# Optimization experiments

Measured on AMD Instinct MI355X. Metric: run time of the kernel, lower is better.

## Reference

```python
import jax, jax.numpy as jnp
import numpy as np

TEMPERATURE = 0.1  # from __init__ temperature
NEG_INF = -1e30


def setup_inputs() -> dict:
    key = jax.random.key(0)
    k1, k2, k3, k4, k5 = jax.random.split(key, 5)
    B, D = 8192, 128
    return {
        "zis": jax.random.normal(k1, (B, D), dtype=jnp.float32),
        "zjs": jax.random.normal(k2, (B, D), dtype=jnp.float32),
        "ilabels": jax.random.randint(k3, (B,), 0, 100, dtype=jnp.int64),
        "jlabels": jax.random.randint(k4, (B,), 0, 100, dtype=jnp.int64),
        "weights": jax.random.uniform(k5, (B,), dtype=jnp.float32),
        "idx": 0,
    }


def reference(zis, zjs, ilabels, jlabels, weights, idx):
    B = zjs.shape[0]
    # forward F.normalize + cosine_matrix's normalize is idempotent -> single L2 normalize
    zi = zis / jnp.linalg.norm(zis, axis=1, keepdims=True)
    zj = zjs / jnp.linalg.norm(zjs, axis=1, keepdims=True)
    # similarity_matrix = 1 - (1 - zj @ zi^T); rows indexed by zjs
    logits = (zj @ zi.T) / TEMPERATURE  # [B, B]
    # labels[i, j] = (ilabels[j] == jlabels[i])
    labels = ilabels[None, :] == jlabels[:, None]  # [B, B] bool
    neg_mask = ~labels  # 'zeros' columns per row
    rows = jnp.arange(B)
    pos_idx = idx + rows  # class_level=False: ones = idx + i, size = 1
    pos = logits[rows, pos_idx]  # [B]
    # CrossEntropy over cat([pos, logits[i, zeros]]) at label 0:
    # loss_i = logsumexp([pos_i, neg_row_i]) - pos_i (numerically stable)
    neg_max = jnp.max(jnp.where(neg_mask, logits, NEG_INF), axis=1)
    m = jnp.maximum(pos, neg_max)  # [B]
    denom = jnp.exp(pos - m) + jnp.sum(
        jnp.where(neg_mask, jnp.exp(logits - m[:, None]), 0.0), axis=1
    )
    loss = m + jnp.log(denom) - pos  # [B]
    # size==1 path: loss*w / w (faithful to torch weighted sum / weight.sum())
    w = weights[pos_idx]
    loss = (loss * w) / w
    return jnp.sum(loss) / B
```

## Files before the change

kernel.cpp:

```cpp
#include <hip/hip_runtime.h>


#define BB 8192
#define DD 128
#define TM 128
#define TN 128
#define NJ 8

typedef __attribute__((ext_vector_type(8))) short short8;
typedef __attribute__((ext_vector_type(4))) float floatx4;

#define GLOBAL_AS __attribute__((address_space(1)))
#define LDS_AS    __attribute__((address_space(3)))

static __device__ __forceinline__ float wave_sum(float v) {
#pragma unroll
    for (int off = 32; off > 0; off >>= 1) v += __shfl_xor(v, off, 64);
    return v;
}

static __device__ __forceinline__ unsigned short f2bf(float f) {
    unsigned int u = __float_as_uint(f);
    return (unsigned short)((u + 0x7FFFu + ((u >> 16) & 1u)) >> 16);
}

__global__ __launch_bounds__(256) void prep_kernel(
    const float* __restrict__ zis, const float* __restrict__ zjs,
    unsigned short* __restrict__ Zib, unsigned short* __restrict__ Zjb,
    float* __restrict__ rni, float* __restrict__ rnj,
    float* __restrict__ denom, float* __restrict__ out, int nout)
{
    if (threadIdx.x < 2) denom[blockIdx.x * 2 + threadIdx.x] = 0.0f;
    if (blockIdx.x == 0 && (int)threadIdx.x < nout) out[threadIdx.x] = 0.0f;

    int wave = threadIdx.x >> 6, lane = threadIdx.x & 63;
    int row = blockIdx.x * 4 + wave;
    const float* src; unsigned short* dst; float* rn; int r;
    if (row < BB) { src = zis; dst = Zib; rn = rni; r = row; }
    else          { src = zjs; dst = Zjb; rn = rnj; r = row - BB; }
    float2 u = *(const float2*)(src + (size_t)r * DD + lane * 2);
    float s = wave_sum(u.x * u.x + u.y * u.y);
    float sc = 1.0f / sqrtf(s);
    if (lane == 0) rn[r] = sc;
    ushort2 o; o.x = f2bf(u.x * sc); o.y = f2bf(u.y * sc);
    *(ushort2*)(dst + (size_t)r * DD + lane * 2) = o;
}

__global__ __launch_bounds__(512, 2) void mfma_tile_kernel(
    const unsigned short* __restrict__ Zjb,
    const unsigned short* __restrict__ Zib,
    const int* __restrict__ ilab, const int* __restrict__ jlab,
    float* __restrict__ denom)
{
    __shared__ __align__(16) unsigned short Bt[2][TN * DD];
    __shared__ int ilds[NJ * TN];

    int tid  = threadIdx.x;
    int lane = tid & 63, wave = tid >> 6;
    int wm = wave >> 1, wn = wave & 1;
    int quad = lane >> 4, l15 = lane & 15;
    int i0    = blockIdx.y * TM;
    int jbase = blockIdx.x * (NJ * TN);

    ilds[tid]       = ilab[jbase + tid];
    ilds[tid + 512] = ilab[jbase + tid + 512];

    int jrv[8];
#pragma unroll
    for (int mt = 0; mt < 2; ++mt)
#pragma unroll
        for (int r = 0; r < 4; ++r)
            jrv[mt * 4 + r] = jlab[i0 + wm * 32 + mt * 16 + quad * 4 + r];

    short8 af[2][4];
#pragma unroll
    for (int mt = 0; mt < 2; ++mt)
#pragma unroll
        for (int ks = 0; ks < 4; ++ks)
            af[mt][ks] = *(const short8*)(Zjb
                + (size_t)(i0 + wm * 32 + mt * 16 + l15) * DD
                + ks * 32 + quad * 8);

    int rl = lane >> 4, p = lane & 15;
    auto stage = [&](int t) {
        const unsigned short* src = Zib + (size_t)(jbase + t * TN) * DD;
        unsigned short* lb = &Bt[t & 1][0];
#pragma unroll
        for (int u = 0; u < 4; ++u) {
            int g = wave * 4 + u;
            int grow = g * 4 + rl;
            int gslot = p ^ (grow & 15);
            const unsigned short* gp = src + (size_t)grow * DD + gslot * 8;
            unsigned short* lp = lb + g * 512;
            __builtin_amdgcn_global_load_lds((const GLOBAL_AS void*)gp,
                                             (LDS_AS void*)lp, 16, 0, 0);
        }
    };

    float rs[2][4];
#pragma unroll
    for (int mt = 0; mt < 2; ++mt)
#pragma unroll
        for (int r = 0; r < 4; ++r) rs[mt][r] = 0.0f;

    auto gran = [&](const unsigned short* bb, int nt, floatx4 (&aC)[2]) {
        int n = wn * 64 + nt * 16 + l15;
#pragma unroll
        for (int ks = 0; ks < 4; ++ks) {
            int ps = (((ks << 2) | quad) ^ l15) << 3;
            short8 b = *(const short8*)(bb + n * DD + ps);
            if (ks == 0) {
                floatx4 zz = (floatx4){0.f, 0.f, 0.f, 0.f};
                aC[0] = __builtin_amdgcn_mfma_f32_16x16x32_bf16(af[0][0], b, zz, 0, 0, 0);
                aC[1] = __builtin_amdgcn_mfma_f32_16x16x32_bf16(af[1][0], b, zz, 0, 0, 0);
            } else {
                aC[0] = __builtin_amdgcn_mfma_f32_16x16x32_bf16(af[0][ks], b, aC[0], 0, 0, 0);
                aC[1] = __builtin_amdgcn_mfma_f32_16x16x32_bf16(af[1][ks], b, aC[1], 0, 0, 0);
            }
        }
    };
    auto epi = [&](floatx4 (&aP)[2], int ilP) {
#pragma unroll
        for (int mt = 0; mt < 2; ++mt)
#pragma unroll
            for (int r = 0; r < 4; ++r) {
                float e = __expf(fmaf(aP[mt][r], 10.0f, -10.0f));
                rs[mt][r] += (ilP != jrv[mt * 4 + r]) ? e : 0.0f;
            }
    };

    floatx4 accA[2], accB[2];
    accB[0] = (floatx4){-1e30f, -1e30f, -1e30f, -1e30f};
    accB[1] = accB[0];
    int ilB = 0;

    stage(0);
    stage(1);
    asm volatile("s_waitcnt vmcnt(4) lgkmcnt(0)" ::: "memory");
    __builtin_amdgcn_s_barrier();

#pragma unroll 2
    for (int t = 0; t < NJ; ++t) {
        const unsigned short* bb = &Bt[t & 1][0];
        const int* ilr = &ilds[t * TN + wn * 64 + l15];
        __builtin_amdgcn_s_setprio(1);
        gran(bb, 0, accA); int il0 = ilr[0];  epi(accB, ilB);
        gran(bb, 1, accB); int il1 = ilr[16]; epi(accA, il0);
        gran(bb, 2, accA); int il2 = ilr[32]; epi(accB, il1);
        gran(bb, 3, accB); ilB = ilr[48];     epi(accA, il2);
        __builtin_amdgcn_s_setprio(0);
        if (t + 1 < NJ) {
            asm volatile("s_waitcnt vmcnt(0)" ::: "memory");
            __builtin_amdgcn_s_barrier();
            if (t + 2 < NJ) stage(t + 2);
        }
    }
    epi(accB, ilB);

#pragma unroll
    for (int mt = 0; mt < 2; ++mt)
#pragma unroll
        for (int r = 0; r < 4; ++r) {
            float v = rs[mt][r];
            v += __shfl_xor(v, 1, 64);
            v += __shfl_xor(v, 2, 64);
            v += __shfl_xor(v, 4, 64);
            v += __shfl_xor(v, 8, 64);
            if (l15 == 0)
                atomicAdd(&denom[i0 + wm * 32 + mt * 16 + quad * 4 + r], v);
        }
}

__global__ __launch_bounds__(256) void posfinal_kernel(
    const float* __restrict__ zis, const float* __restrict__ zjs,
    const float* __restrict__ rni, const float* __restrict__ rnj,
    const float* __restrict__ denom, const float* __restrict__ wts,
    const int* __restrict__ idxp, float* __restrict__ out)
{
    int wave = threadIdx.x >> 6, lane = threadIdx.x & 63;
    int idx = idxp[0];
    float ll = 0.0f;
#pragma unroll
    for (int t = 0; t < 4; ++t) {
        int i = blockIdx.x * 16 + wave * 4 + t;
        int j = idx + i;
        float2 a  = *(const float2*)(zjs + (size_t)i * DD + lane * 2);
        float2 b2 = *(const float2*)(zis + (size_t)j * DD + lane * 2);
        float s = wave_sum(a.x * b2.x + a.y * b2.y);
        if (lane == 0) {
            float p = s * rni[j] * rnj[i] * 10.0f;
            float l = 10.0f + logf(__expf(p - 10.0f) + denom[i]) - p;
            float w = wts[j];
            ll += (l * w) / w;
        }
    }
    __shared__ float part[4];
    if (lane == 0) part[wave] = ll;
    __syncthreads();
    if (threadIdx.x == 0)
        atomicAdd(out, (part[0] + part[1] + part[2] + part[3]) * (1.0f / BB));
}

extern "C" void kernel_launch(void* const* d_in, const int* in_sizes, int n_in,
                              void* d_out, int out_size, void* d_ws, size_t ws_size,
                              hipStream_t stream) {
    const float* zis = (const float*)d_in[0];
    const float* zjs = (const float*)d_in[1];
    const int* ilab = (const int*)d_in[2];
    const int* jlab = (const int*)d_in[3];
    const float* wts = (const float*)d_in[4];
    const int* idxp = (const int*)d_in[5];
    float* out = (float*)d_out;

    float* rni   = (float*)d_ws;
    float* rnj   = rni + BB;
    float* denom = rnj + BB;
    unsigned short* Zib = (unsigned short*)(denom + BB);
    unsigned short* Zjb = Zib + (size_t)BB * DD;

    prep_kernel<<<2 * BB / 4, 256, 0, stream>>>(
        zis, zjs, Zib, Zjb, rni, rnj, denom, out, out_size);
    mfma_tile_kernel<<<dim3(BB / (NJ * TN), BB / TM), 512, 0, stream>>>(
        Zjb, Zib, ilab, jlab, denom);
    posfinal_kernel<<<BB / 16, 256, 0, stream>>>(
        zis, zjs, rni, rnj, denom, wts, idxp, out);
}
```

Measured before the change: 116.5 us.

## Replace LDS-staged tile GEMM with register-direct per-wave strip kernel

```diff
diff --git a/kernel.cpp b/kernel.cpp
--- a/kernel.cpp
+++ b/kernel.cpp
@@ -3,15 +3,12 @@
 
 #define BB 8192
 #define DD 128
-#define TM 128
-#define TN 128
-#define NJ 8
+#define RW 32
+#define CW 512
+#define NG (CW / 16)
 
 typedef __attribute__((ext_vector_type(8))) short short8;
 typedef __attribute__((ext_vector_type(4))) float floatx4;
-
-#define GLOBAL_AS __attribute__((address_space(1)))
-#define LDS_AS    __attribute__((address_space(3)))
 
 static __device__ __forceinline__ float wave_sum(float v) {
 #pragma unroll
@@ -46,31 +43,19 @@
     *(ushort2*)(dst + (size_t)r * DD + lane * 2) = o;
 }
 
-__global__ __launch_bounds__(512, 2) void mfma_tile_kernel(
+__global__ __launch_bounds__(256, 4) void dot_kernel(
     const unsigned short* __restrict__ Zjb,
     const unsigned short* __restrict__ Zib,
     const int* __restrict__ ilab, const int* __restrict__ jlab,
     float* __restrict__ denom)
 {
-    __shared__ __align__(16) unsigned short Bt[2][TN * DD];
-    __shared__ int ilds[NJ * TN];
+    int lane = threadIdx.x & 63, wave = threadIdx.x >> 6;
+    int quad = lane >> 4, l15 = lane & 15;
 
-    int tid  = threadIdx.x;
-    int lane = tid & 63, wave = tid >> 6;
-    int wm = wave >> 1, wn = wave & 1;
-    int quad = lane >> 4, l15 = lane & 15;
-    int i0    = blockIdx.y * TM;
-    int jbase = blockIdx.x * (NJ * TN);
-
-    ilds[tid]       = ilab[jbase + tid];
-    ilds[tid + 512] = ilab[jbase + tid + 512];
-
-    int jrv[8];
-#pragma unroll
-    for (int mt = 0; mt < 2; ++mt)
-#pragma unroll
-        for (int r = 0; r < 4; ++r)
-            jrv[mt * 4 + r] = jlab[i0 + wm * 32 + mt * 16 + quad * 4 + r];
+    int cc = blockIdx.x >> 6;
+    int rg = ((blockIdx.x & 63) << 2) + wave;
+    int r0 = rg * RW;
+    int c0 = cc * CW;
 
     short8 af[2][4];
 #pragma unroll
@@ -78,24 +63,14 @@
 #pragma unroll
         for (int ks = 0; ks < 4; ++ks)
             af[mt][ks] = *(const short8*)(Zjb
-                + (size_t)(i0 + wm * 32 + mt * 16 + l15) * DD
-                + ks * 32 + quad * 8);
+                + (size_t)(r0 + mt * 16 + l15) * DD + ks * 32 + quad * 8);
 
-    int rl = lane >> 4, p = lane & 15;
-    auto stage = [&](int t) {
-        const unsigned short* src = Zib + (size_t)(jbase + t * TN) * DD;
-        unsigned short* lb = &Bt[t & 1][0];
+    int jrv[8];
 #pragma unroll
-        for (int u = 0; u < 4; ++u) {
-            int g = wave * 4 + u;
-            int grow = g * 4 + rl;
-            int gslot = p ^ (grow & 15);
-            const unsigned short* gp = src + (size_t)grow * DD + gslot * 8;
-            unsigned short* lp = lb + g * 512;
-            __builtin_amdgcn_global_load_lds((const GLOBAL_AS void*)gp,
-                                             (LDS_AS void*)lp, 16, 0, 0);
-        }
-    };
+    for (int mt = 0; mt < 2; ++mt)
+#pragma unroll
+        for (int r = 0; r < 4; ++r)
+            jrv[mt * 4 + r] = jlab[r0 + mt * 16 + quad * 4 + r];
 
     float rs[2][4];
 #pragma unroll
@@ -103,59 +78,54 @@
 #pragma unroll
         for (int r = 0; r < 4; ++r) rs[mt][r] = 0.0f;
 
-    auto gran = [&](const unsigned short* bb, int nt, floatx4 (&aC)[2]) {
-        int n = wn * 64 + nt * 16 + l15;
+    const unsigned short* bp = Zib + (size_t)(c0 + l15) * DD + quad * 8;
+    const int* ilp = ilab + c0 + l15;
+
+    auto LD = [&](short8 (&b)[4], int g) {
+        const unsigned short* q = bp + (size_t)g * (16 * DD);
+        b[0] = *(const short8*)(q);
+        b[1] = *(const short8*)(q + 32);
+        b[2] = *(const short8*)(q + 64);
+        b[3] = *(const short8*)(q + 96);
+    };
+    auto GRAN = [&](short8 (&b)[4], floatx4 (&a)[2]) {
+        floatx4 zz = (floatx4){0.f, 0.f, 0.f, 0.f};
+        a[0] = __builtin_amdgcn_mfma_f32_16x16x32_bf16(af[0][0], b[0], zz, 0, 0, 0);
+        a[1] = __builtin_amdgcn_mfma_f32_16x16x32_bf16(af[1][0], b[0], zz, 0, 0, 0);
 #pragma unroll
-        for (int ks = 0; ks < 4; ++ks) {
-            int ps = (((ks << 2) | quad) ^ l15) << 3;
-            short8 b = *(const short8*)(bb + n * DD + ps);
-            if (ks == 0) {
-                floatx4 zz = (floatx4){0.f, 0.f, 0.f, 0.f};
-                aC[0] = __builtin_amdgcn_mfma_f32_16x16x32_bf16(af[0][0], b, zz, 0, 0, 0);
-                aC[1] = __builtin_amdgcn_mfma_f32_16x16x32_bf16(af[1][0], b, zz, 0, 0, 0);
-            } else {
-                aC[0] = __builtin_amdgcn_mfma_f32_16x16x32_bf16(af[0][ks], b, aC[0], 0, 0, 0);
-                aC[1] = __builtin_amdgcn_mfma_f32_16x16x32_bf16(af[1][ks], b, aC[1], 0, 0, 0);
-            }
+        for (int ks = 1; ks < 4; ++ks) {
+            a[0] = __builtin_amdgcn_mfma_f32_16x16x32_bf16(af[0][ks], b[ks], a[0], 0, 0, 0);
+            a[1] = __builtin_amdgcn_mfma_f32_16x16x32_bf16(af[1][ks], b[ks], a[1], 0, 0, 0);
         }
     };
-    auto epi = [&](floatx4 (&aP)[2], int ilP) {
+    auto EPI = [&](floatx4 (&a)[2], int il) {
 #pragma unroll
         for (int mt = 0; mt < 2; ++mt)
 #pragma unroll
             for (int r = 0; r < 4; ++r) {
-                float e = __expf(fmaf(aP[mt][r], 10.0f, -10.0f));
-                rs[mt][r] += (ilP != jrv[mt * 4 + r]) ? e : 0.0f;
+                float e = __expf(fmaf(a[mt][r], 10.0f, -10.0f));
+                rs[mt][r] += (il != jrv[mt * 4 + r]) ? e : 0.0f;
             }
     };
 
+    short8 b0[4], b1[4];
     floatx4 accA[2], accB[2];
     accB[0] = (floatx4){-1e30f, -1e30f, -1e30f, -1e30f};
     accB[1] = accB[0];
-    int ilB = 0;
+    int ilA = 0, ilB = 0;
 
-    stage(0);
-    stage(1);
-    asm volatile("s_waitcnt vmcnt(4) lgkmcnt(0)" ::: "memory");
-    __builtin_amdgcn_s_barrier();
+    LD(b0, 0);
+    int iln0 = ilp[0], iln1 = 0;
 
-#pragma unroll 2
-    for (int t = 0; t < NJ; ++t) {
-        const unsigned short* bb = &Bt[t & 1][0];
-        const int* ilr = &ilds[t * TN + wn * 64 + l15];
-        __builtin_amdgcn_s_setprio(1);
-        gran(bb, 0, accA); int il0 = ilr[0];  epi(accB, ilB);
-        gran(bb, 1, accB); int il1 = ilr[16]; epi(accA, il0);
-        gran(bb, 2, accA); int il2 = ilr[32]; epi(accB, il1);
-        gran(bb, 3, accB); ilB = ilr[48];     epi(accA, il2);
-        __builtin_amdgcn_s_setprio(0);
-        if (t + 1 < NJ) {
-            asm volatile("s_waitcnt vmcnt(0)" ::: "memory");
-            __builtin_amdgcn_s_barrier();
-            if (t + 2 < NJ) stage(t + 2);
-        }
+    for (int g = 0; g < NG; g += 2) {
+        if (g + 1 < NG) { LD(b1, g + 1); iln1 = ilp[(g + 1) * 16]; }
+        GRAN(b0, accA); ilA = iln0;
+        EPI(accB, ilB);
+        if (g + 2 < NG) { LD(b0, g + 2); iln0 = ilp[(g + 2) * 16]; }
+        GRAN(b1, accB); ilB = iln1;
+        EPI(accA, ilA);
     }
-    epi(accB, ilB);
+    EPI(accB, ilB);
 
 #pragma unroll
     for (int mt = 0; mt < 2; ++mt)
@@ -167,7 +137,7 @@
             v += __shfl_xor(v, 4, 64);
             v += __shfl_xor(v, 8, 64);
             if (l15 == 0)
-                atomicAdd(&denom[i0 + wm * 32 + mt * 16 + quad * 4 + r], v);
+                atomicAdd(&denom[r0 + mt * 16 + quad * 4 + r], v);
         }
 }
 
@@ -220,7 +190,7 @@
 
     prep_kernel<<<2 * BB / 4, 256, 0, stream>>>(
         zis, zjs, Zib, Zjb, rni, rnj, denom, out, out_size);
-    mfma_tile_kernel<<<dim3(BB / (NJ * TN), BB / TM), 512, 0, stream>>>(
+    dot_kernel<<<(BB / RW / 4) * (BB / CW), 256, 0, stream>>>(
         Zjb, Zib, ilab, jlab, denom);
     posfinal_kernel<<<BB / 16, 256, 0, stream>>>(
         zis, zjs, rni, rnj, denom, wts, idxp, out);
```

New measurement: 144.8 us. 1.24x slower.
